# Kernel tuning notes

Measured on AMD Instinct MI355X. Metric: run time of the kernel, lower is better.

The kernel has to match this reference:

```python
import jax, jax.numpy as jnp
import numpy as np
from jax import lax

_RGB2XYZ = np.array([[0.412453, 0.357580, 0.180423],
                     [0.212671, 0.715160, 0.072169],
                     [0.019334, 0.119193, 0.950227]], dtype=np.float32)
_XYZ_REF = np.array([0.95047, 1.0, 1.08883], dtype=np.float32)


def rgb_to_lab(img):
    # img: [B,3,H,W] sRGB in [0,1] (kornia convention)
    lin = jnp.where(img > 0.04045, ((img + 0.055) / 1.055) ** 2.4, img / 12.92)
    xyz = jnp.einsum('ij,bjhw->bihw', jnp.asarray(_RGB2XYZ), lin)
    xyz = xyz / jnp.asarray(_XYZ_REF)[None, :, None, None]
    f = jnp.where(xyz > 0.008856, jnp.cbrt(xyz), 7.787 * xyz + 4.0 / 29.0)
    fx, fy, fz = f[:, 0], f[:, 1], f[:, 2]
    return jnp.stack([116.0 * fy - 16.0, 500.0 * (fx - fy), 200.0 * (fy - fz)], axis=1)


def grid_sample_border(img, gx, gy):
    # bilinear grid_sample, padding_mode='border', align_corners=False
    # img [B,C,H,W]; gx, gy normalized coords [B,H,W]
    B, C, H, W = img.shape
    x = jnp.clip(((gx + 1.0) * W - 1.0) * 0.5, 0.0, W - 1.0)
    y = jnp.clip(((gy + 1.0) * H - 1.0) * 0.5, 0.0, H - 1.0)
    x0 = jnp.floor(x); y0 = jnp.floor(y)
    wx = x - x0; wy = y - y0
    x0i = x0.astype(jnp.int32); y0i = y0.astype(jnp.int32)
    x1i = jnp.minimum(x0i + 1, W - 1); y1i = jnp.minimum(y0i + 1, H - 1)

    def one(im, x0i, x1i, y0i, y1i, wx, wy):
        g = lambda yy, xx: im[:, yy, xx]  # [C,H,W] gather
        top = g(y0i, x0i) * (1 - wx) + g(y0i, x1i) * wx
        bot = g(y1i, x0i) * (1 - wx) + g(y1i, x1i) * wx
        return top * (1 - wy) + bot * wy

    return jax.vmap(one)(img, x0i, x1i, y0i, y1i, wx, wy)


def backward_warp(img, flow):
    # flow channels are (dy, dx); q = 2*flow/[H,W] + identity grid in [-1,1]
    B, _, H, W = flow.shape
    base_y = jnp.linspace(-1.0, 1.0, H, dtype=flow.dtype)[None, :, None]
    base_x = jnp.linspace(-1.0, 1.0, W, dtype=flow.dtype)[None, None, :]
    gy = 2.0 * flow[:, 0] / H + base_y
    gx = 2.0 * flow[:, 1] / W + base_x
    return grid_sample_border(img, gx, gy)


def softsplat_softmax(inp, flow, metric):
    # softmax splatting: inp [B,C,H,W], flow [B,2,H,W] as (dx,dy), metric [B,1,H,W]
    w = jnp.exp(metric)
    inp = jnp.concatenate([inp * w, w], axis=1)  # [B,C+1,H,W]
    B, C, H, W = inp.shape
    fx = flow[:, 0] + jnp.arange(W, dtype=flow.dtype)[None, None, :]
    fy = flow[:, 1] + jnp.arange(H, dtype=flow.dtype)[None, :, None]
    x0i = jnp.floor(fx).astype(jnp.int32)
    y0i = jnp.floor(fy).astype(jnp.int32)
    idxs, wgts = [], []
    for dx, dy in ((0, 0), (1, 0), (0, 1), (1, 1)):
        xi = x0i + dx; yi = y0i + dy
        wgt = (1.0 - jnp.abs(fx - xi.astype(fx.dtype))) * (1.0 - jnp.abs(fy - yi.astype(fy.dtype)))
        valid = (xi >= 0) & (xi < W) & (yi >= 0) & (yi < H)
        idxs.append((jnp.clip(yi, 0, H - 1) * W + jnp.clip(xi, 0, W - 1)).reshape(B, -1))
        wgts.append((wgt * valid).reshape(B, -1))
    idxs = jnp.stack(idxs, 0)  # [4,B,HW]
    wgts = jnp.stack(wgts, 0)

    def splat_one(inp_b, idx4, wgt4):  # inp_b [C,H,W]
        flat = inp_b.reshape(C, -1)
        out = jnp.zeros_like(flat)
        for c in range(4):
            out = out.at[:, idx4[c]].add(flat * wgt4[c][None, :])
        return out.reshape(C, H, W)

    out = jax.vmap(splat_one, in_axes=(0, 1, 1))(inp, idxs, wgts)
    norm = out[:, -1:]
    norm = jnp.where(norm == 0.0, 1.0, norm)
    return out[:, :-1] / norm


def forward_warp(img, flow, metric):
    # append ones mask channel; flip flow (dy,dx)->(dx,dy) as in forward_warpping
    B, _, H, W = img.shape
    img_m = jnp.concatenate([img, jnp.ones((B, 1, H, W), img.dtype)], axis=1)
    return softsplat_softmax(img_m, flow[:, ::-1], metric)


def morph_open(x, k):
    # erosion (min-pool) then dilation (max-pool), k x k, stride 1, pad k//2
    p = k // 2
    pad = [(0, 0), (0, 0), (p, p), (p, p)]
    er = lax.reduce_window(x, jnp.asarray(np.inf, x.dtype), lax.min, (1, 1, k, k), (1, 1, 1, 1), pad)
    return lax.reduce_window(er, jnp.asarray(-np.inf, x.dtype), lax.max, (1, 1, k, k), (1, 1, 1, 1), pad)


def z_metric(I0, I1, flow0to1, flow1to0):
    lab0 = rgb_to_lab(I0)
    lab1 = rgb_to_lab(I1)
    z1to0 = -0.1 * jnp.linalg.norm(lab1 - backward_warp(lab0, flow1to0), axis=1, keepdims=True)
    z0to1 = -0.1 * jnp.linalg.norm(lab0 - backward_warp(lab1, flow0to1), axis=1, keepdims=True)
    return z0to1, z1to0


def setup_inputs() -> dict:
    key = jax.random.key(0)
    k0, k1, k2, k3 = jax.random.split(key, 4)
    B, C, H, W = 4, 3, 1024, 1024
    return {
        'I0': jax.random.uniform(k0, (B, C, H, W), dtype=jnp.float32),
        'I1': jax.random.uniform(k1, (B, C, H, W), dtype=jnp.float32),
        'flow0to1': jax.random.normal(k2, (B, 2, H, W), dtype=jnp.float32) * 8.0,
        'flow1to0': jax.random.normal(k3, (B, 2, H, W), dtype=jnp.float32) * 8.0,
        'morph_kernel_size': 5,
    }


def reference(I0, I1, flow0to1, flow1to0, morph_kernel_size):
    z0to1, z1to0 = z_metric(I0, I1, flow0to1, flow1to0)
    # tau is None -> flow0tot = flow0to1, flow1tot = flow1to0
    fw0 = forward_warp(I0, flow0to1, z0to1)  # [B,4,H,W] (rgb + splat mask)
    fw1 = forward_warp(I1, flow1to0, z1to0)
    w0, w1 = fw0[:, :-1], fw1[:, :-1]
    m0 = morph_open(fw0[:, -1:], morph_kernel_size)
    m1 = morph_open(fw1[:, -1:], morph_kernel_size)
    base0 = jnp.concatenate([m0 * w0 + (1 - m0) * w1, m0], axis=1)
    base1 = jnp.concatenate([m1 * w1 + (1 - m1) * w0, m1], axis=1)
    return base0, base1
```

## Files before the change

### kernel.cpp

```cpp
#include <hip/hip_runtime.h>

#define NB 4
#define NH 1024
#define NW 1024
#define NHW (NH * NW)

#define TS 32
#define HP 16
#define SRCS 64
#define SRC_PX (SRCS * SRCS)
#define TILE_PX (TS * TS)

__device__ __forceinline__ float srgb2lin(float v) {
    return v > 0.04045f ? powf((v + 0.055f) * (1.0f / 1.055f), 2.4f) : v * (1.0f / 12.92f);
}

__device__ __forceinline__ float labf(float t) {
    return t > 0.008856f ? cbrtf(t) : 7.787f * t + 4.0f / 29.0f;
}

__global__ void lab_kernel(const float* __restrict__ I0, const float* __restrict__ I1,
                           float4* __restrict__ lab0, float4* __restrict__ lab1) {
    int idx = blockIdx.x * blockDim.x + threadIdx.x;
    const int total = 2 * NB * NHW;
    if (idx >= total) return;
    int img = (idx >= NB * NHW) ? 1 : 0;
    int p = idx - img * NB * NHW;
    int b = p / NHW;
    int hw = p - b * NHW;
    const float* src = (img ? I1 : I0) + (size_t)b * 3 * NHW + hw;
    float4* dst = (img ? lab1 : lab0) + ((size_t)b * NHW + hw);

    float r = srgb2lin(src[0]);
    float g = srgb2lin(src[NHW]);
    float bl = srgb2lin(src[2 * NHW]);

    float X = (0.412453f * r + 0.35758f * g + 0.180423f * bl) * (1.0f / 0.95047f);
    float Y = (0.212671f * r + 0.71516f * g + 0.072169f * bl);
    float Z = (0.019334f * r + 0.119193f * g + 0.950227f * bl) * (1.0f / 1.08883f);

    float fx = labf(X);
    float fy = labf(Y);
    float fz = labf(Z);

    *dst = make_float4(116.0f * fy - 16.0f, 500.0f * (fx - fy), 200.0f * (fy - fz), 0.0f);
}

__global__ __launch_bounds__(256) void wmap_kernel(
        const float4* __restrict__ lab0, const float4* __restrict__ lab1,
        const float* __restrict__ I0, const float* __restrict__ I1,
        const float* __restrict__ f01, const float* __restrict__ f10,
        float4* __restrict__ pm0, float4* __restrict__ pm1) {
    const int z = blockIdx.z;
    const int dir = z >> 2;
    const int b = z & (NB - 1);
    const int tx = threadIdx.x & 31;
    const int ty = threadIdx.x >> 5;
    const int x = blockIdx.x * 32 + tx;
    const int y = blockIdx.y * 8 + ty;
    const int hw = y * NW + x;

    const float4* la  = (dir ? lab1 : lab0) + (size_t)b * NHW;
    const float4* lb  = (dir ? lab0 : lab1) + (size_t)b * NHW;
    const float* img = (dir ? I1 : I0) + (size_t)b * 3 * NHW;
    const float* fb  = (dir ? f10 : f01) + (size_t)b * 2 * NHW;
    float4* pm = (dir ? pm1 : pm0) + (size_t)b * NHW;

    const float fy_d = fb[hw];
    const float fx_d = fb[NHW + hw];

    float base_y = -1.0f + 2.0f * (float)y / (float)(NH - 1);
    float base_x = -1.0f + 2.0f * (float)x / (float)(NW - 1);
    float gy = 2.0f * fy_d / (float)NH + base_y;
    float gx = 2.0f * fx_d / (float)NW + base_x;
    float ys = fminf(fmaxf(((gy + 1.0f) * (float)NH - 1.0f) * 0.5f, 0.0f), (float)(NH - 1));
    float xs = fminf(fmaxf(((gx + 1.0f) * (float)NW - 1.0f) * 0.5f, 0.0f), (float)(NW - 1));
    float y0f = floorf(ys), x0f = floorf(xs);
    int y0 = (int)y0f, x0 = (int)x0f;
    int y1 = min(y0 + 1, NH - 1), x1 = min(x0 + 1, NW - 1);
    float wy = ys - y0f, wx = xs - x0f;

    const float4 p00 = lb[y0 * NW + x0];
    const float4 p01 = lb[y0 * NW + x1];
    const float4 p10 = lb[y1 * NW + x0];
    const float4 p11 = lb[y1 * NW + x1];
    const float4 pa  = la[hw];

    float3 top, bot, v;
    top.x = p00.x * (1.0f - wx) + p01.x * wx;
    top.y = p00.y * (1.0f - wx) + p01.y * wx;
    top.z = p00.z * (1.0f - wx) + p01.z * wx;
    bot.x = p10.x * (1.0f - wx) + p11.x * wx;
    bot.y = p10.y * (1.0f - wx) + p11.y * wx;
    bot.z = p10.z * (1.0f - wx) + p11.z * wx;
    v.x = top.x * (1.0f - wy) + bot.x * wy;
    v.y = top.y * (1.0f - wy) + bot.y * wy;
    v.z = top.z * (1.0f - wy) + bot.z * wy;
    float dx_ = pa.x - v.x, dy_ = pa.y - v.y, dz_ = pa.z - v.z;
    float ss = dx_ * dx_ + dy_ * dy_ + dz_ * dz_;
    float w = expf(-0.1f * sqrtf(ss));

    pm[hw] = make_float4(img[hw] * w, img[NHW + hw] * w, img[2 * NHW + hw] * w, w);
}

__global__ __launch_bounds__(1024, 2) void splat_bin_kernel(
        const float4* __restrict__ pm0, const float4* __restrict__ pm1,
        const float* __restrict__ f01, const float* __restrict__ f10,
        float4* __restrict__ acc4,
        float4* __restrict__ ovf) {
    __shared__ unsigned       head[33 * 33];
    __shared__ unsigned short nxt[SRC_PX];
    __shared__ float2         flows[SRC_PX];

    const int t = threadIdx.x;
    const int z = blockIdx.z;
    const int dir = z >> 2;
    const int b = z & (NB - 1);
    const int tx0 = blockIdx.x * TS;
    const int ty0 = blockIdx.y * TS;
    const int ox = tx0 - HP;
    const int oy = ty0 - HP;

    for (int i = t; i < 33 * 33; i += 1024) head[i] = 0xFFFFu;
    __syncthreads();

    const float4* pm = (dir ? pm1 : pm0) + (size_t)b * NHW;
    const float* fb  = (dir ? f10 : f01) + (size_t)b * 2 * NHW;
    float4* a4 = acc4 + ((size_t)dir * NB + b) * NHW;
    float4* ov = ovf  + ((size_t)dir * NB + b) * NHW;

#pragma unroll
    for (int kk = 0; kk < 4; ++kk) {
        const int i = t + kk * 1024;
        const int rx = i & (SRCS - 1);
        const int ry = i >> 6;
        const int sx = ox + rx;
        const int sy = oy + ry;
        if (sx < 0 || sx >= NW || sy < 0 || sy >= NH) continue;
        const int hw = sy * NW + sx;

        const float fy_d = fb[hw];
        const float fx_d = fb[NHW + hw];
        flows[i] = make_float2(fx_d, fy_d);

        const float px = fx_d + (float)sx;
        const float py = fy_d + (float)sy;
        const int fcx = (int)floorf(px);
        const int fcy = (int)floorf(py);
        const int mx = fcx - tx0;
        const int my = fcy - ty0;

        if (mx >= -1 && mx < TS && my >= -1 && my < TS) {
            unsigned old = atomicExch(&head[(my + 1) * 33 + (mx + 1)], (unsigned)i);
            nxt[i] = (unsigned short)old;
        }

        const bool interior = (rx >= HP) && (rx < HP + TS) && (ry >= HP) && (ry < HP + TS);
        if (interior) {
            float4 p4; bool loaded = false;
#pragma unroll
            for (int dy = 0; dy < 2; ++dy) {
                const int yi = fcy + dy;
                if (yi < 0 || yi >= NH) continue;
                const float wgy = 1.0f - fabsf(py - (float)yi);
#pragma unroll
                for (int dx = 0; dx < 2; ++dx) {
                    const int xi = fcx + dx;
                    if (xi < 0 || xi >= NW) continue;
                    const int ttx0 = xi & ~(TS - 1);
                    const int tty0 = yi & ~(TS - 1);
                    const bool covered = (sx >= ttx0 - HP) && (sx < ttx0 + TS + HP) &&
                                         (sy >= tty0 - HP) && (sy < tty0 + TS + HP);
                    if (!covered) {
                        if (!loaded) { p4 = pm[hw]; loaded = true; }
                        const float wg = wgy * (1.0f - fabsf(px - (float)xi));
                        float* p = (float*)(ov + (yi * NW + xi));
                        atomicAdd(p + 0, p4.x * wg);
                        atomicAdd(p + 1, p4.y * wg);
                        atomicAdd(p + 2, p4.z * wg);
                        atomicAdd(p + 3, p4.w * wg);
                    }
                }
            }
        }
    }
    __syncthreads();

    {
        const int lx = t & (TS - 1);
        const int ly = t >> 5;
        const int cx = tx0 + lx;
        const int cy = ty0 + ly;
        const float cxf = (float)cx;
        const float cyf = (float)cy;

        float sx_ = 0.0f, sy_ = 0.0f, sz_ = 0.0f, sw_ = 0.0f;

#pragma unroll
        for (int dy = 0; dy < 2; ++dy) {
#pragma unroll
            for (int dx = 0; dx < 2; ++dx) {
                unsigned e = head[(ly + 1 - dy) * 33 + (lx + 1 - dx)];
                int guard = SRC_PX;
                while (e != 0xFFFFu && --guard >= 0) {
                    const float2 f = flows[e];
                    const int rx = e & (SRCS - 1);
                    const int ry = (int)e >> 6;
                    const int sxx = ox + rx;
                    const int syy = oy + ry;
                    const float px = f.x + (float)sxx;
                    const float py = f.y + (float)syy;
                    const float wg = (1.0f - fabsf(px - cxf)) * (1.0f - fabsf(py - cyf));
                    const float4 p4 = pm[syy * NW + sxx];
                    sx_ += p4.x * wg;
                    sy_ += p4.y * wg;
                    sz_ += p4.z * wg;
                    sw_ += p4.w * wg;
                    e = nxt[e];
                }
            }
        }
        a4[cy * NW + cx] = make_float4(sx_, sy_, sz_, sw_);
    }
}

__global__ __launch_bounds__(256) void merge_kernel(
        float4* __restrict__ acc4, const float4* __restrict__ ovf,
        float* __restrict__ wpl) {
    const size_t total = (size_t)2 * NB * NHW;
    for (size_t i = (size_t)blockIdx.x * blockDim.x + threadIdx.x; i < total;
         i += (size_t)gridDim.x * blockDim.x) {
        float4 a = acc4[i];
        float4 o = ovf[i];
        a.x += o.x; a.y += o.y; a.z += o.z; a.w += o.w;
        acc4[i] = a;
        wpl[i] = a.w;
    }
}

__global__ __launch_bounds__(256) void morph_compose_kernel(
        const float4* __restrict__ acc4, const float* __restrict__ wpl,
        float* __restrict__ out, const int* __restrict__ kptr) {
    __shared__ float bufOA[64 * 64], bufOB[64 * 64];
    __shared__ float bufHA[64 * 48], bufHB[64 * 48];

    const int t = threadIdx.x;
    const int b = blockIdx.z;
    const int x0 = blockIdx.x * 32;
    const int y0 = blockIdx.y * 32;
    const int k = *kptr;
    const int p = k >> 1;

    const float* wa = wpl + (size_t)b * NHW;
    const float* wb = wpl + ((size_t)NB + b) * NHW;

    float mA[4], mB[4];

    if (p <= 8) {
        const int OS = 32 + 4 * p;
        const int ES = 32 + 2 * p;
        const int KW = 2 * p + 1;
        for (int i = t; i < OS * OS; i += 256) {
            int sx = x0 - 2 * p + (i % OS);
            int sy = y0 - 2 * p + (i / OS);
            float oa = 1.0f, ob = 1.0f;
            if (sx >= 0 && sx < NW && sy >= 0 && sy < NH) {
                int o = sy * NW + sx;
                oa = (wa[o] != 0.0f) ? 1.0f : 0.0f;
                ob = (wb[o] != 0.0f) ? 1.0f : 0.0f;
            }
            bufOA[i] = oa; bufOB[i] = ob;
        }
        __syncthreads();
        for (int i = t; i < OS * ES; i += 256) {
            int y = i / ES, x = i % ES;
            float ma = 1.0f, mb = 1.0f;
            for (int d = 0; d < KW; ++d) {
                ma = fminf(ma, bufOA[y * OS + x + d]);
                mb = fminf(mb, bufOB[y * OS + x + d]);
            }
            bufHA[i] = ma; bufHB[i] = mb;
        }
        __syncthreads();
        for (int i = t; i < ES * ES; i += 256) {
            int ly = i / ES, lx = i % ES;
            int ex = x0 - p + lx, ey = y0 - p + ly;
            float ea = 0.0f, eb = 0.0f;
            if (ex >= 0 && ex < NW && ey >= 0 && ey < NH) {
                ea = 1.0f; eb = 1.0f;
                for (int d = 0; d < KW; ++d) {
                    ea = fminf(ea, bufHA[(ly + d) * ES + lx]);
                    eb = fminf(eb, bufHB[(ly + d) * ES + lx]);
                }
            }
            bufOA[i] = ea; bufOB[i] = eb;
        }
        __syncthreads();
        for (int i = t; i < ES * 32; i += 256) {
            int y = i >> 5, x = i & 31;
            float ma = 0.0f, mb = 0.0f;
            for (int d = 0; d < KW; ++d) {
                ma = fmaxf(ma, bufOA[y * ES + x + d]);
                mb = fmaxf(mb, bufOB[y * ES + x + d]);
            }
            bufHA[i] = ma; bufHB[i] = mb;
        }
        __syncthreads();
#pragma unroll
        for (int r = 0; r < 4; ++r) {
            int lx = t & 31, ly = (t >> 5) + r * 8;
            float ma = 0.0f, mb = 0.0f;
            for (int d = 0; d < KW; ++d) {
                ma = fmaxf(ma, bufHA[((ly + d) << 5) + lx]);
                mb = fmaxf(mb, bufHB[((ly + d) << 5) + lx]);
            }
            mA[r] = ma; mB[r] = mb;
        }
    } else {
#pragma unroll
        for (int r = 0; r < 4; ++r) {
            int x = x0 + (t & 31), y = y0 + (t >> 5) + r * 8;
            float ma = 0.0f, mb = 0.0f;
            for (int dy2 = -p; dy2 <= p; ++dy2) {
                int qy = y + dy2; if (qy < 0 || qy >= NH) continue;
                for (int dx2 = -p; dx2 <= p; ++dx2) {
                    int qx = x + dx2; if (qx < 0 || qx >= NW) continue;
                    if (ma >= 1.0f && mb >= 1.0f) break;
                    float ea = 1.0f, eb = 1.0f;
                    for (int dy = -p; dy <= p; ++dy) {
                        int yy = qy + dy; if (yy < 0 || yy >= NH) continue;
                        for (int dx = -p; dx <= p; ++dx) {
                            int xx = qx + dx; if (xx < 0 || xx >= NW) continue;
                            int o = yy * NW + xx;
                            if (wa[o] == 0.0f) ea = 0.0f;
                            if (wb[o] == 0.0f) eb = 0.0f;
                        }
                    }
                    ma = fmaxf(ma, ea);
                    mb = fmaxf(mb, eb);
                }
            }
            mA[r] = ma; mB[r] = mb;
        }
    }

    const float4* a0 = acc4 + (size_t)b * NHW;
    const float4* a1 = acc4 + ((size_t)NB + b) * NHW;
    float* o0 = out + (size_t)b * 4 * NHW;
    float* o1 = out + (size_t)NB * 4 * NHW + (size_t)b * 4 * NHW;

#pragma unroll
    for (int r = 0; r < 4; ++r) {
        int lx = t & 31, ly = (t >> 5) + r * 8;
        int x = x0 + lx, y = y0 + ly;
        int hw = y * NW + x;
        float4 v0 = a0[hw];
        float4 v1 = a1[hw];
        float d0 = (v0.w == 0.0f) ? 1.0f : v0.w;
        float d1 = (v1.w == 0.0f) ? 1.0f : v1.w;
        float m0 = mA[r], m1 = mB[r];
        float w00 = v0.x / d0, w01 = v0.y / d0, w02 = v0.z / d0;
        float w10 = v1.x / d1, w11 = v1.y / d1, w12 = v1.z / d1;
        o0[hw]           = m0 * w00 + (1.0f - m0) * w10;
        o0[NHW + hw]     = m0 * w01 + (1.0f - m0) * w11;
        o0[2 * NHW + hw] = m0 * w02 + (1.0f - m0) * w12;
        o0[3 * NHW + hw] = m0;
        o1[hw]           = m1 * w10 + (1.0f - m1) * w00;
        o1[NHW + hw]     = m1 * w11 + (1.0f - m1) * w01;
        o1[2 * NHW + hw] = m1 * w12 + (1.0f - m1) * w02;
        o1[3 * NHW + hw] = m1;
    }
}

extern "C" void kernel_launch(void* const* d_in, const int* in_sizes, int n_in,
                              void* d_out, int out_size, void* d_ws, size_t ws_size,
                              hipStream_t stream) {
    const float* I0  = (const float*)d_in[0];
    const float* I1  = (const float*)d_in[1];
    const float* f01 = (const float*)d_in[2];
    const float* f10 = (const float*)d_in[3];
    const int*  kptr = (const int*)d_in[4];

    float* ws = (float*)d_ws;
    const size_t n = (size_t)NB * NHW;
    float4* pm0   = (float4*)ws;
    float4* pm1   = (float4*)(ws + 4 * n);
    float*  wpl   = ws;
    float4* lab40 = (float4*)(ws + 8 * n);
    float4* lab41 = (float4*)(ws + 12 * n);
    float4* acc4  = (float4*)(ws + 8 * n);
    float4* ovf   = (float4*)d_out;

    const int T = 256;
    int gLab = (2 * NB * NHW + T - 1) / T;
    dim3 gW(NW / 32, NH / 8, 2 * NB);
    dim3 gTile(NW / TS, NH / TS, 2 * NB);
    dim3 gCmp(NW / 32, NH / 32, NB);

    hipMemsetAsync(d_out, 0, 8 * n * sizeof(float), stream);
    lab_kernel<<<gLab, T, 0, stream>>>(I0, I1, lab40, lab41);
    wmap_kernel<<<gW, T, 0, stream>>>(lab40, lab41, I0, I1, f01, f10, pm0, pm1);
    splat_bin_kernel<<<gTile, 1024, 0, stream>>>(pm0, pm1, f01, f10, acc4, ovf);
    merge_kernel<<<4096, T, 0, stream>>>(acc4, ovf, wpl);
    morph_compose_kernel<<<gCmp, T, 0, stream>>>(acc4, wpl, (float*)d_out, kptr);
}
```

Measured before the change: 751.0 us.

## Drop merge kernel by accumulating splats directly into planar output with atomics

Removes the separate merge pass. The splat kernel now atomically adds its per-tile sums straight into the planar output buffer, with weights going to a separate plane. The compose kernel then normalizes and blends in place, which avoids the float4 accumulator round trip and the merge read/write traffic. The overflow scan is skipped for sources whose flow magnitude is at most 15, since those always land inside the 16-pixel halo. This costs atomic stores on every non-empty pixel and an extra memset of the weight planes.

```diff
diff --git a/kernel.cpp b/kernel.cpp
--- a/kernel.cpp
+++ b/kernel.cpp
@@ -106,8 +106,8 @@
 __global__ __launch_bounds__(1024, 2) void splat_bin_kernel(
         const float4* __restrict__ pm0, const float4* __restrict__ pm1,
         const float* __restrict__ f01, const float* __restrict__ f10,
-        float4* __restrict__ acc4,
-        float4* __restrict__ ovf) {
+        float* __restrict__ out,
+        float* __restrict__ wpl) {
     __shared__ unsigned       head[33 * 33];
     __shared__ unsigned short nxt[SRC_PX];
     __shared__ float2         flows[SRC_PX];
@@ -126,8 +126,8 @@
 
     const float4* pm = (dir ? pm1 : pm0) + (size_t)b * NHW;
     const float* fb  = (dir ? f10 : f01) + (size_t)b * 2 * NHW;
-    float4* a4 = acc4 + ((size_t)dir * NB + b) * NHW;
-    float4* ov = ovf  + ((size_t)dir * NB + b) * NHW;
+    float* od = out + ((size_t)dir * NB + b) * 4 * NHW;
+    float* wv = wpl + ((size_t)dir * NB + b) * NHW;
 
 #pragma unroll
     for (int kk = 0; kk < 4; ++kk) {
@@ -156,7 +156,7 @@
         }
 
         const bool interior = (rx >= HP) && (rx < HP + TS) && (ry >= HP) && (ry < HP + TS);
-        if (interior) {
+        if (interior && fmaxf(fabsf(fx_d), fabsf(fy_d)) > 15.0f) {
             float4 p4; bool loaded = false;
 #pragma unroll
             for (int dy = 0; dy < 2; ++dy) {
@@ -174,11 +174,11 @@
                     if (!covered) {
                         if (!loaded) { p4 = pm[hw]; loaded = true; }
                         const float wg = wgy * (1.0f - fabsf(px - (float)xi));
-                        float* p = (float*)(ov + (yi * NW + xi));
-                        atomicAdd(p + 0, p4.x * wg);
-                        atomicAdd(p + 1, p4.y * wg);
-                        atomicAdd(p + 2, p4.z * wg);
-                        atomicAdd(p + 3, p4.w * wg);
+                        const int o = yi * NW + xi;
+                        atomicAdd(od + o,           p4.x * wg);
+                        atomicAdd(od + NHW + o,     p4.y * wg);
+                        atomicAdd(od + 2 * NHW + o, p4.z * wg);
+                        atomicAdd(wv + o,           p4.w * wg);
                     }
                 }
             }
@@ -220,27 +220,18 @@
                 }
             }
         }
-        a4[cy * NW + cx] = make_float4(sx_, sy_, sz_, sw_);
+        if (sw_ != 0.0f) {
+            const int o = cy * NW + cx;
+            atomicAdd(od + o,           sx_);
+            atomicAdd(od + NHW + o,     sy_);
+            atomicAdd(od + 2 * NHW + o, sz_);
+            atomicAdd(wv + o,           sw_);
+        }
     }
 }
 
-__global__ __launch_bounds__(256) void merge_kernel(
-        float4* __restrict__ acc4, const float4* __restrict__ ovf,
-        float* __restrict__ wpl) {
-    const size_t total = (size_t)2 * NB * NHW;
-    for (size_t i = (size_t)blockIdx.x * blockDim.x + threadIdx.x; i < total;
-         i += (size_t)gridDim.x * blockDim.x) {
-        float4 a = acc4[i];
-        float4 o = ovf[i];
-        a.x += o.x; a.y += o.y; a.z += o.z; a.w += o.w;
-        acc4[i] = a;
-        wpl[i] = a.w;
-    }
-}
-
 __global__ __launch_bounds__(256) void morph_compose_kernel(
-        const float4* __restrict__ acc4, const float* __restrict__ wpl,
-        float* __restrict__ out, const int* __restrict__ kptr) {
+        const float* __restrict__ wpl, float* out, const int* __restrict__ kptr) {
     __shared__ float bufOA[64 * 64], bufOB[64 * 64];
     __shared__ float bufHA[64 * 48], bufHB[64 * 48];
 
@@ -344,8 +335,6 @@
         }
     }
 
-    const float4* a0 = acc4 + (size_t)b * NHW;
-    const float4* a1 = acc4 + ((size_t)NB + b) * NHW;
     float* o0 = out + (size_t)b * 4 * NHW;
     float* o1 = out + (size_t)NB * 4 * NHW + (size_t)b * 4 * NHW;
 
@@ -354,13 +343,15 @@
         int lx = t & 31, ly = (t >> 5) + r * 8;
         int x = x0 + lx, y = y0 + ly;
         int hw = y * NW + x;
-        float4 v0 = a0[hw];
-        float4 v1 = a1[hw];
-        float d0 = (v0.w == 0.0f) ? 1.0f : v0.w;
-        float d1 = (v1.w == 0.0f) ? 1.0f : v1.w;
+        float n0 = wa[hw];
+        float n1 = wb[hw];
+        float d0 = (n0 == 0.0f) ? 1.0f : n0;
+        float d1 = (n1 == 0.0f) ? 1.0f : n1;
+        float c00 = o0[hw], c01 = o0[NHW + hw], c02 = o0[2 * NHW + hw];
+        float c10 = o1[hw], c11 = o1[NHW + hw], c12 = o1[2 * NHW + hw];
         float m0 = mA[r], m1 = mB[r];
-        float w00 = v0.x / d0, w01 = v0.y / d0, w02 = v0.z / d0;
-        float w10 = v1.x / d1, w11 = v1.y / d1, w12 = v1.z / d1;
+        float w00 = c00 / d0, w01 = c01 / d0, w02 = c02 / d0;
+        float w10 = c10 / d1, w11 = c11 / d1, w12 = c12 / d1;
         o0[hw]           = m0 * w00 + (1.0f - m0) * w10;
         o0[NHW + hw]     = m0 * w01 + (1.0f - m0) * w11;
         o0[2 * NHW + hw] = m0 * w02 + (1.0f - m0) * w12;
@@ -385,11 +376,9 @@
     const size_t n = (size_t)NB * NHW;
     float4* pm0   = (float4*)ws;
     float4* pm1   = (float4*)(ws + 4 * n);
-    float*  wpl   = ws;
     float4* lab40 = (float4*)(ws + 8 * n);
     float4* lab41 = (float4*)(ws + 12 * n);
-    float4* acc4  = (float4*)(ws + 8 * n);
-    float4* ovf   = (float4*)d_out;
+    float*  wpl   = ws + 8 * n;
 
     const int T = 256;
     int gLab = (2 * NB * NHW + T - 1) / T;
@@ -400,7 +389,7 @@
     hipMemsetAsync(d_out, 0, 8 * n * sizeof(float), stream);
     lab_kernel<<<gLab, T, 0, stream>>>(I0, I1, lab40, lab41);
     wmap_kernel<<<gW, T, 0, stream>>>(lab40, lab41, I0, I1, f01, f10, pm0, pm1);
-    splat_bin_kernel<<<gTile, 1024, 0, stream>>>(pm0, pm1, f01, f10, acc4, ovf);
-    merge_kernel<<<4096, T, 0, stream>>>(acc4, ovf, wpl);
-    morph_compose_kernel<<<gCmp, T, 0, stream>>>(acc4, wpl, (float*)d_out, kptr);
-}
+    hipMemsetAsync(wpl, 0, 2 * n * sizeof(float), stream);
+    splat_bin_kernel<<<gTile, 1024, 0, stream>>>(pm0, pm1, f01, f10, (float*)d_out, wpl);
+    morph_compose_kernel<<<gCmp, T, 0, stream>>>(wpl, (float*)d_out, kptr);
+}
```

New measurement: 741.3 us. About the same (-1.3%).
